# Kernel optimization log

Hardware: AMD Instinct MI355X
Metric: run time of the kernel (lower is better)

Reference implementation:

```python
import jax, jax.numpy as jnp
import numpy as np
import math
from jax import lax

_EPS = 1e-8


def _sinkhorn_uv(M, iters):
    # M: [BL, N, N] positive. Returns diagonal entries u, v of U, V such that
    # diag(u) @ M @ diag(v) is (approximately) doubly stochastic.
    u = jnp.ones(M.shape[:-1], M.dtype)  # [BL, N]
    v = jnp.ones(M.shape[:-1], M.dtype)  # [BL, N]
    def body(carry, _):
        u, v = carry
        u = 1.0 / (jnp.einsum('bij,bj->bi', M, v) + _EPS)
        v = 1.0 / (jnp.einsum('bij,bi->bj', M, u) + _EPS)
        return (u, v), None
    (u, v), _ = lax.scan(body, (u, v), None, length=iters)
    return u, v


def setup_inputs() -> dict:
    key = jax.random.key(0)
    k1, k2, k3, k4 = jax.random.split(key, 4)
    B, L, N, D = 2, 2048, 4, 2048
    nc = N * D
    nout = N * N + 2 * N
    h = jax.random.normal(k1, (B, L, N, D), dtype=jnp.float32)
    gamma = jnp.ones((nc,), dtype=jnp.float32)
    w = jax.random.normal(k2, (nc, nout), dtype=jnp.float32) * 0.02
    alpha = jnp.ones((3,), dtype=jnp.float32) * 0.01 + jax.random.uniform(k3, (3,)) * 0.01
    beta = jax.random.normal(k4, (nout,), dtype=jnp.float32) * 0.01
    return {"h": h, "gamma": gamma, "w": w, "alpha": alpha, "beta": beta, "max_sk_it": 10}


def reference(h, gamma, w, alpha, beta, max_sk_it):
    B, L, N, D = h.shape
    nc = N * D
    # --- mapping ---
    h_flat = h.reshape(B, L, nc)
    h_vec = gamma * h_flat                      # RMSNorm gamma scaling (module skips the division here)
    H = jnp.einsum('blc,co->blo', h_vec, w)     # [B, L, N^2 + 2N]
    r = jnp.linalg.norm(h_flat, axis=-1, keepdims=True) / math.sqrt(nc)
    r_ = 1.0 / r
    H_pre = jax.nn.sigmoid(r_ * H[..., :N] * alpha[0] + beta[:N])                 # [B,L,N]
    H_post = 2.0 * jax.nn.sigmoid(r_ * H[..., N:2 * N] * alpha[1] + beta[N:2 * N])  # [B,L,N]
    H_res_lin = r_ * H[..., 2 * N:] * alpha[2] + beta[2 * N:]                      # [B,L,N*N]
    M = jnp.exp(H_res_lin).reshape(B * L, N, N)
    u, v = _sinkhorn_uv(M, max_sk_it)
    u = lax.stop_gradient(u)
    v = lax.stop_gradient(v)
    P = u[:, :, None] * M * v[:, None, :]       # U @ M @ V with diagonal U, V
    H_res = P.reshape(B, L, N, N)
    # --- process ---
    h_pre = jnp.einsum('bln,blnd->bld', H_pre, h)        # [B,L,D]
    h_res = jnp.einsum('blmn,blnd->blmd', H_res, h)      # [B,L,N,D]
    # --- depth_connection (identity residual branch: h_out = h_pre) ---
    out = H_post[..., None] * h_pre[:, :, None, :] + h_res  # [B,L,N,D]
    return out
```

## Files before the change

kernel.cpp:

```cpp
#include <hip/hip_runtime.h>
#include <stdint.h>

#define NC       8192
#define D_       2048
#define NOUTS    24
#define WPAD     8224
#define NB       32
#define KW       512
#define LPAD     520

typedef __attribute__((ext_vector_type(8))) short short8;
typedef __attribute__((ext_vector_type(4))) float f32x4;

__device__ __forceinline__ uint16_t f32_to_bf16_bits(float f) {
    uint32_t u = __builtin_bit_cast(uint32_t, f);
    return (uint16_t)((u + 0x7FFFu + ((u >> 16) & 1u)) >> 16);
}


__global__ void prep_wb_kernel(const float* __restrict__ w,
                               const float* __restrict__ gamma,
                               uint16_t* __restrict__ wb) {
    int idx = blockIdx.x * blockDim.x + threadIdx.x;
    if (idx >= NB * NC) return;
    int o = idx / NC;
    int c = idx - o * NC;
    float v = (o < NOUTS) ? gamma[c] * w[c * NOUTS + o] : 0.0f;
    wb[o * NC + c] = f32_to_bf16_bits(v);
}

__global__ __launch_bounds__(256, 4) void gemv_mfma_lds_kernel(
    const float* __restrict__ h, const uint16_t* __restrict__ wb,
    float* __restrict__ part, int nrows)
{
    __shared__ __align__(16) uint16_t lwb[32][LPAD];

    const int tid  = threadIdx.x;
    const int lane = tid & 63;
    const int wid  = tid >> 6;
    const int nrg  = nrows >> 4;
    const int s    = (blockIdx.x * 4) / nrg;
    const int k0   = s * KW;

    {
        const int row = tid >> 3;
        const int col = (tid & 7) << 6;
        const uint16_t* src = wb + (size_t)row * NC + k0 + col;
        uint16_t* dst = &lwb[row][col];
#pragma unroll
        for (int i = 0; i < 8; ++i)
            *reinterpret_cast<uint4*>(dst + i * 8) =
                *reinterpret_cast<const uint4*>(src + i * 8);
    }
    __syncthreads();

    const int rg   = (blockIdx.x * 4 + wid) % nrg;
    const int r0   = rg * 16;
    const int arow = lane & 15;
    const int kgrp = (lane >> 4) << 3;
    const float*    hA  = h + (size_t)(r0 + arow) * NC + k0 + kgrp;
    const uint16_t* lB0 = &lwb[arow][kgrp];
    const uint16_t* lB1 = &lwb[arow + 16][kgrp];

    f32x4 acc0 = {0.f, 0.f, 0.f, 0.f};
    f32x4 acc1 = {0.f, 0.f, 0.f, 0.f};
    float ss = 0.0f;

#pragma unroll 8
    for (int k = 0; k < KW; k += 32) {
        const float4 a_lo = *reinterpret_cast<const float4*>(hA + k);
        const float4 a_hi = *reinterpret_cast<const float4*>(hA + k + 4);
        const short8 b0 = *reinterpret_cast<const short8*>(lB0 + k);
        const short8 b1 = *reinterpret_cast<const short8*>(lB1 + k);

        ss += a_lo.x*a_lo.x + a_lo.y*a_lo.y + a_lo.z*a_lo.z + a_lo.w*a_lo.w
            + a_hi.x*a_hi.x + a_hi.y*a_hi.y + a_hi.z*a_hi.z + a_hi.w*a_hi.w;

        short8 av;
        av[0] = (short)f32_to_bf16_bits(a_lo.x);
        av[1] = (short)f32_to_bf16_bits(a_lo.y);
        av[2] = (short)f32_to_bf16_bits(a_lo.z);
        av[3] = (short)f32_to_bf16_bits(a_lo.w);
        av[4] = (short)f32_to_bf16_bits(a_hi.x);
        av[5] = (short)f32_to_bf16_bits(a_hi.y);
        av[6] = (short)f32_to_bf16_bits(a_hi.z);
        av[7] = (short)f32_to_bf16_bits(a_hi.w);

        acc0 = __builtin_amdgcn_mfma_f32_16x16x32_bf16(av, b0, acc0, 0, 0, 0);
        acc1 = __builtin_amdgcn_mfma_f32_16x16x32_bf16(av, b1, acc1, 0, 0, 0);
    }

    ss += __shfl_xor(ss, 16, 64);
    ss += __shfl_xor(ss, 32, 64);

    const int o0   = lane & 15;
    const int crow = r0 + ((lane >> 4) << 2);
    float* pbase = part + (size_t)s * 25 * nrows;
#pragma unroll
    for (int i = 0; i < 4; ++i)
        pbase[(size_t)o0 * nrows + crow + i] = acc0[i];
    if (o0 < NOUTS - 16) {
#pragma unroll
        for (int i = 0; i < 4; ++i)
            pbase[(size_t)(o0 + 16) * nrows + crow + i] = acc1[i];
    }
    if (lane < 16)
        pbase[(size_t)24 * nrows + r0 + lane] = ss;
}

__global__ __launch_bounds__(256, 4) void gemv_mfma_kernel(
    const float* __restrict__ h, const uint16_t* __restrict__ wb,
    float* __restrict__ part, int nrows, int nslices)
{
    const int lane = threadIdx.x & 63;
    const int unit = blockIdx.x * 4 + (threadIdx.x >> 6);
    const int nrg  = nrows >> 4;
    const int rg   = unit % nrg;
    const int s    = unit / nrg;
    if (s >= nslices) return;
    const int r0 = rg * 16;
    const int kw = NC / nslices;
    const int k0 = s * kw;

    const int arow = lane & 15;
    const int kgrp = (lane >> 4) << 3;
    const float*    hA  = h  + (size_t)(r0 + arow) * NC + k0 + kgrp;
    const uint16_t* wB0 = wb + (size_t)arow        * NC + k0 + kgrp;
    const uint16_t* wB1 = wb + (size_t)(arow + 16) * NC + k0 + kgrp;

    f32x4 acc0 = {0.f, 0.f, 0.f, 0.f};
    f32x4 acc1 = {0.f, 0.f, 0.f, 0.f};
    float ss = 0.0f;

#pragma unroll 4
    for (int k = 0; k < kw; k += 32) {
        const float4 a_lo = *reinterpret_cast<const float4*>(hA + k);
        const float4 a_hi = *reinterpret_cast<const float4*>(hA + k + 4);
        const short8 b0 = *reinterpret_cast<const short8*>(wB0 + k);
        const short8 b1 = *reinterpret_cast<const short8*>(wB1 + k);

        ss += a_lo.x*a_lo.x + a_lo.y*a_lo.y + a_lo.z*a_lo.z + a_lo.w*a_lo.w
            + a_hi.x*a_hi.x + a_hi.y*a_hi.y + a_hi.z*a_hi.z + a_hi.w*a_hi.w;

        short8 av;
        av[0] = (short)f32_to_bf16_bits(a_lo.x);
        av[1] = (short)f32_to_bf16_bits(a_lo.y);
        av[2] = (short)f32_to_bf16_bits(a_lo.z);
        av[3] = (short)f32_to_bf16_bits(a_lo.w);
        av[4] = (short)f32_to_bf16_bits(a_hi.x);
        av[5] = (short)f32_to_bf16_bits(a_hi.y);
        av[6] = (short)f32_to_bf16_bits(a_hi.z);
        av[7] = (short)f32_to_bf16_bits(a_hi.w);

        acc0 = __builtin_amdgcn_mfma_f32_16x16x32_bf16(av, b0, acc0, 0, 0, 0);
        acc1 = __builtin_amdgcn_mfma_f32_16x16x32_bf16(av, b1, acc1, 0, 0, 0);
    }

    ss += __shfl_xor(ss, 16, 64);
    ss += __shfl_xor(ss, 32, 64);

    const int o0   = lane & 15;
    const int crow = r0 + ((lane >> 4) << 2);
    float* pbase = part + (size_t)s * 25 * nrows;
#pragma unroll
    for (int i = 0; i < 4; ++i)
        pbase[(size_t)o0 * nrows + crow + i] = acc0[i];
    if (o0 < NOUTS - 16) {
#pragma unroll
        for (int i = 0; i < 4; ++i)
            pbase[(size_t)(o0 + 16) * nrows + crow + i] = acc1[i];
    }
    if (lane < 16)
        pbase[(size_t)24 * nrows + r0 + lane] = ss;
}

__global__ void sinkhorn_wave_kernel(const float* __restrict__ part,
                                     const float* __restrict__ alpha,
                                     const float* __restrict__ beta,
                                     const int* __restrict__ it_ptr,
                                     float* __restrict__ Cbuf, int nrows, int nslices)
{
    const int lane = threadIdx.x & 63;
    const int row  = blockIdx.x * 4 + (threadIdx.x >> 6);
    if (row >= nrows) return;

    const int o = lane & 31;
    const int g = lane >> 5;
    float acc = 0.0f;
    if (o < 25) {
#pragma unroll 4
        for (int s = g; s < nslices; s += 2)
            acc += part[((size_t)s * 25 + o) * nrows + row];
    }
    acc += __shfl_xor(acc, 32, 64);

    float H[25];
#pragma unroll
    for (int i = 0; i < 25; ++i) H[i] = __shfl(acc, i, 64);

    const float r_ = sqrtf((float)NC / H[24]);
    const float a0 = alpha[0], a1 = alpha[1], a2 = alpha[2];

    float Hpre[4], Hpost[4], M[16];
#pragma unroll
    for (int n = 0; n < 4; ++n) {
        const float x = r_ * H[n] * a0 + beta[n];
        Hpre[n] = __builtin_amdgcn_rcpf(1.0f + __expf(-x));
        const float y = r_ * H[4 + n] * a1 + beta[4 + n];
        Hpost[n] = 2.0f * __builtin_amdgcn_rcpf(1.0f + __expf(-y));
    }
#pragma unroll
    for (int k = 0; k < 16; ++k)
        M[k] = __expf(r_ * H[8 + k] * a2 + beta[8 + k]);

    float u[4] = {1.f, 1.f, 1.f, 1.f}, vv[4] = {1.f, 1.f, 1.f, 1.f};
    int iters = *it_ptr;
    if (iters < 0 || iters > 10000) {
        const float f = __int_as_float(iters);
        iters = (f >= 0.0f && f < 10000.0f) ? (int)f : 10;
    }
    for (int it = 0; it < iters; ++it) {
#pragma unroll
        for (int i = 0; i < 4; ++i)
            u[i] = __builtin_amdgcn_rcpf(
                M[4*i+0]*vv[0] + M[4*i+1]*vv[1] + M[4*i+2]*vv[2] + M[4*i+3]*vv[3] + 1e-8f);
#pragma unroll
        for (int j2 = 0; j2 < 4; ++j2)
            vv[j2] = __builtin_amdgcn_rcpf(
                M[j2]*u[0] + M[4+j2]*u[1] + M[8+j2]*u[2] + M[12+j2]*u[3] + 1e-8f);
    }

    if (lane < 16) {
        const int m = lane >> 2, n = lane & 3;
        Cbuf[(size_t)row * 16 + lane] = Hpost[m] * Hpre[n] + u[m] * M[lane] * vv[n];
    }
}

__global__ __launch_bounds__(256, 8) void mix_kernel(
    const float* __restrict__ h, const float* __restrict__ Cbuf,
    float* __restrict__ out)
{
    const int row = blockIdx.x;
    const float* cr = Cbuf + (size_t)row * 16;
    float C[16];
#pragma unroll
    for (int k = 0; k < 16; ++k) C[k] = cr[k];

    const float* hr = h + (size_t)row * NC;
    float* orow = out + (size_t)row * NC;
#pragma unroll
    for (int t = 0; t < 2; ++t) {
        const int d0 = t * 1024 + (threadIdx.x << 2);
        float4 hn[4];
#pragma unroll
        for (int n = 0; n < 4; ++n)
            hn[n] = *reinterpret_cast<const float4*>(hr + n * D_ + d0);
#pragma unroll
        for (int m = 0; m < 4; ++m) {
            float4 o4;
            o4.x = C[4*m+0]*hn[0].x + C[4*m+1]*hn[1].x + C[4*m+2]*hn[2].x + C[4*m+3]*hn[3].x;
            o4.y = C[4*m+0]*hn[0].y + C[4*m+1]*hn[1].y + C[4*m+2]*hn[2].y + C[4*m+3]*hn[3].y;
            o4.z = C[4*m+0]*hn[0].z + C[4*m+1]*hn[1].z + C[4*m+2]*hn[2].z + C[4*m+3]*hn[3].z;
            o4.w = C[4*m+0]*hn[0].w + C[4*m+1]*hn[1].w + C[4*m+2]*hn[2].w + C[4*m+3]*hn[3].w;
            *reinterpret_cast<float4*>(orow + m * D_ + d0) = o4;
        }
    }
}


__global__ void prep_w_kernel(const float* __restrict__ w, float* __restrict__ wp) {
    int idx = blockIdx.x * blockDim.x + threadIdx.x;
    if (idx >= NOUTS * NC) return;
    int o = idx / NC;
    int c = idx - o * NC;
    wp[o * WPAD + c] = w[c * NOUTS + o];
}

__global__ __launch_bounds__(256, 4) void fused_kernel(
    const float* __restrict__ h, const float* __restrict__ gamma,
    const float* __restrict__ wp, const float* __restrict__ alpha,
    const float* __restrict__ beta, const int* __restrict__ it_ptr,
    float* __restrict__ out, int nrows)
{
    const int wave = threadIdx.x >> 6;
    const int lane = threadIdx.x & 63;
    const int row  = (blockIdx.x << 2) | wave;
    if (row >= nrows) return;
    const float* hrow = h + (size_t)row * NC;

    float acc[NOUTS];
#pragma unroll
    for (int o = 0; o < NOUTS; ++o) acc[o] = 0.0f;
    float sumsq = 0.0f;
    const int base = lane << 2;
#pragma unroll 2
    for (int j = 0; j < 32; ++j) {
        const int c0 = base + (j << 8);
        const float4 h4 = *reinterpret_cast<const float4*>(hrow + c0);
        const float4 g4 = *reinterpret_cast<const float4*>(gamma + c0);
        sumsq += h4.x*h4.x + h4.y*h4.y + h4.z*h4.z + h4.w*h4.w;
        const float v0 = h4.x*g4.x, v1 = h4.y*g4.y, v2 = h4.z*g4.z, v3 = h4.w*g4.w;
#pragma unroll
        for (int o = 0; o < NOUTS; ++o) {
            const float4 w4 = *reinterpret_cast<const float4*>(wp + o * WPAD + c0);
            acc[o] += v0*w4.x + v1*w4.y + v2*w4.z + v3*w4.w;
        }
    }
#pragma unroll
    for (int m = 1; m < 64; m <<= 1) {
        sumsq += __shfl_xor(sumsq, m, 64);
#pragma unroll
        for (int o = 0; o < NOUTS; ++o) acc[o] += __shfl_xor(acc[o], m, 64);
    }
    const float r_ = sqrtf((float)NC / sumsq);
    const float a0 = alpha[0], a1 = alpha[1], a2 = alpha[2];
    float Hpre[4], Hpost[4], M[16];
#pragma unroll
    for (int n = 0; n < 4; ++n) {
        const float x = r_ * acc[n] * a0 + beta[n];
        Hpre[n] = __builtin_amdgcn_rcpf(1.0f + __expf(-x));
        const float y = r_ * acc[4 + n] * a1 + beta[4 + n];
        Hpost[n] = 2.0f * __builtin_amdgcn_rcpf(1.0f + __expf(-y));
    }
#pragma unroll
    for (int k = 0; k < 16; ++k)
        M[k] = __expf(r_ * acc[8 + k] * a2 + beta[8 + k]);
    float u[4] = {1.f,1.f,1.f,1.f}, v[4] = {1.f,1.f,1.f,1.f};
    int iters = *it_ptr;
    if (iters < 0 || iters > 10000) {
        const float f = __int_as_float(iters);
        iters = (f >= 0.0f && f < 10000.0f) ? (int)f : 10;
    }
    for (int it = 0; it < iters; ++it) {
#pragma unroll
        for (int i = 0; i < 4; ++i)
            u[i] = __builtin_amdgcn_rcpf(M[4*i+0]*v[0] + M[4*i+1]*v[1] + M[4*i+2]*v[2] + M[4*i+3]*v[3] + 1e-8f);
#pragma unroll
        for (int j2 = 0; j2 < 4; ++j2)
            v[j2] = __builtin_amdgcn_rcpf(M[j2]*u[0] + M[4+j2]*u[1] + M[8+j2]*u[2] + M[12+j2]*u[3] + 1e-8f);
    }
    float P[16];
#pragma unroll
    for (int i = 0; i < 4; ++i)
#pragma unroll
        for (int j2 = 0; j2 < 4; ++j2)
            P[4*i + j2] = u[i] * M[4*i + j2] * v[j2];
    float* orow = out + (size_t)row * NC;
#pragma unroll 2
    for (int t = 0; t < 8; ++t) {
        const int d0 = base + (t << 8);
        float hn[4][4];
#pragma unroll
        for (int n = 0; n < 4; ++n) {
            const float4 x4 = *reinterpret_cast<const float4*>(hrow + n * D_ + d0);
            hn[n][0]=x4.x; hn[n][1]=x4.y; hn[n][2]=x4.z; hn[n][3]=x4.w;
        }
        float hp[4];
#pragma unroll
        for (int k = 0; k < 4; ++k)
            hp[k] = Hpre[0]*hn[0][k] + Hpre[1]*hn[1][k] + Hpre[2]*hn[2][k] + Hpre[3]*hn[3][k];
#pragma unroll
        for (int m = 0; m < 4; ++m) {
            float4 o4;
            o4.x = Hpost[m]*hp[0] + P[4*m+0]*hn[0][0] + P[4*m+1]*hn[1][0] + P[4*m+2]*hn[2][0] + P[4*m+3]*hn[3][0];
            o4.y = Hpost[m]*hp[1] + P[4*m+0]*hn[0][1] + P[4*m+1]*hn[1][1] + P[4*m+2]*hn[2][1] + P[4*m+3]*hn[3][1];
            o4.z = Hpost[m]*hp[2] + P[4*m+0]*hn[0][2] + P[4*m+1]*hn[1][2] + P[4*m+2]*hn[2][2] + P[4*m+3]*hn[3][2];
            o4.w = Hpost[m]*hp[3] + P[4*m+0]*hn[0][3] + P[4*m+1]*hn[1][3] + P[4*m+2]*hn[2][3] + P[4*m+3]*hn[3][3];
            *reinterpret_cast<float4*>(orow + m * D_ + d0) = o4;
        }
    }
}


extern "C" void kernel_launch(void* const* d_in, const int* in_sizes, int n_in,
                              void* d_out, int out_size, void* d_ws, size_t ws_size,
                              hipStream_t stream) {
    const float* h     = (const float*)d_in[0];
    const float* gamma = (const float*)d_in[1];
    const float* w     = (const float*)d_in[2];
    const float* alpha = (const float*)d_in[3];
    const float* beta  = (const float*)d_in[4];
    const int*   itp   = (const int*)d_in[5];
    float*       out   = (float*)d_out;

    const int nrows = in_sizes[0] / NC;

    const size_t wb_bytes = (size_t)NB * NC * 2;
    const size_t c_bytes  = (size_t)nrows * 16 * 4;

    int nslices = 0;
    if ((nrows % 16) == 0) {
        for (int cand = 16; cand >= 4; cand >>= 1) {
            const size_t pb = (size_t)cand * 25 * nrows * 4;
            if (ws_size >= wb_bytes + pb + c_bytes) { nslices = cand; break; }
        }
    }

    if (nslices) {
        uint16_t* wb   = (uint16_t*)d_ws;
        float*    part = (float*)((char*)d_ws + wb_bytes);
        float*    Cbuf = (float*)((char*)d_ws + wb_bytes + (size_t)nslices * 25 * nrows * 4);

        prep_wb_kernel<<<(NB * NC + 255) / 256, 256, 0, stream>>>(w, gamma, wb);
        if (nslices == 16 && (nrows % 64) == 0) {
            const int units = (nrows / 16) * 16;
            gemv_mfma_lds_kernel<<<units / 4, 256, 0, stream>>>(h, wb, part, nrows);
        } else {
            const int units = (nrows / 16) * nslices;
            gemv_mfma_kernel<<<(units + 3) / 4, 256, 0, stream>>>(h, wb, part, nrows, nslices);
        }
        sinkhorn_wave_kernel<<<(nrows + 3) / 4, 256, 0, stream>>>(part, alpha, beta, itp, Cbuf, nrows, nslices);
        mix_kernel<<<nrows, 256, 0, stream>>>(h, Cbuf, out);
    } else {
        float* wp = (float*)d_ws;
        prep_w_kernel<<<(NOUTS * NC + 255) / 256, 256, 0, stream>>>(w, wp);
        fused_kernel<<<(nrows + 3) / 4, 256, 0, stream>>>(h, gamma, wp, alpha, beta, itp, out, nrows);
    }
}
```

Measured before the change: 98.33 us.

## Fuse Sinkhorn coefficient computation into the mixing kernel per row

Merges the separate Sinkhorn kernel and the mix kernel into one kernel with one block per row. The first wave reduces the GEMV partials, runs Sinkhorn and writes the 16 mixing coefficients to shared memory. Meanwhile all threads have already issued their loads of h, which overlaps the h fetch with the Sinkhorn latency. This removes a kernel launch and the round trip of the coefficient buffer through global memory. In exchange, 63 of every 64 rows of Sinkhorn work sit behind a block-wide barrier, each block spends serial Sinkhorn time, and occupancy is reduced by register pressure.

```diff
diff --git a/kernel.cpp b/kernel.cpp
--- a/kernel.cpp
+++ b/kernel.cpp
@@ -174,96 +174,98 @@
         pbase[(size_t)24 * nrows + r0 + lane] = ss;
 }
 
-__global__ void sinkhorn_wave_kernel(const float* __restrict__ part,
-                                     const float* __restrict__ alpha,
-                                     const float* __restrict__ beta,
-                                     const int* __restrict__ it_ptr,
-                                     float* __restrict__ Cbuf, int nrows, int nslices)
+__global__ __launch_bounds__(256, 4) void sinkmix_kernel(
+    const float* __restrict__ h, const float* __restrict__ part,
+    const float* __restrict__ alpha, const float* __restrict__ beta,
+    const int* __restrict__ it_ptr, float* __restrict__ out,
+    int nrows, int nslices)
 {
-    const int lane = threadIdx.x & 63;
-    const int row  = blockIdx.x * 4 + (threadIdx.x >> 6);
-    if (row >= nrows) return;
-
-    const int o = lane & 31;
-    const int g = lane >> 5;
-    float acc = 0.0f;
-    if (o < 25) {
+    __shared__ float Cs[16];
+    const int row = blockIdx.x;
+    const int tid = threadIdx.x;
+    const float* hr = h + (size_t)row * NC;
+
+    const int d0 = tid << 2;
+    const int d1 = d0 + 1024;
+    float4 hA[4], hB[4];
+#pragma unroll
+    for (int n = 0; n < 4; ++n) {
+        hA[n] = *reinterpret_cast<const float4*>(hr + n * D_ + d0);
+        hB[n] = *reinterpret_cast<const float4*>(hr + n * D_ + d1);
+    }
+
+    if (tid < 64) {
+        const int o = tid & 31;
+        const int g = tid >> 5;
+        float acc = 0.0f;
+        if (o < 25) {
 #pragma unroll 4
-        for (int s = g; s < nslices; s += 2)
-            acc += part[((size_t)s * 25 + o) * nrows + row];
-    }
-    acc += __shfl_xor(acc, 32, 64);
-
-    float H[25];
-#pragma unroll
-    for (int i = 0; i < 25; ++i) H[i] = __shfl(acc, i, 64);
-
-    const float r_ = sqrtf((float)NC / H[24]);
-    const float a0 = alpha[0], a1 = alpha[1], a2 = alpha[2];
-
-    float Hpre[4], Hpost[4], M[16];
-#pragma unroll
-    for (int n = 0; n < 4; ++n) {
-        const float x = r_ * H[n] * a0 + beta[n];
-        Hpre[n] = __builtin_amdgcn_rcpf(1.0f + __expf(-x));
-        const float y = r_ * H[4 + n] * a1 + beta[4 + n];
-        Hpost[n] = 2.0f * __builtin_amdgcn_rcpf(1.0f + __expf(-y));
-    }
-#pragma unroll
-    for (int k = 0; k < 16; ++k)
-        M[k] = __expf(r_ * H[8 + k] * a2 + beta[8 + k]);
-
-    float u[4] = {1.f, 1.f, 1.f, 1.f}, vv[4] = {1.f, 1.f, 1.f, 1.f};
-    int iters = *it_ptr;
-    if (iters < 0 || iters > 10000) {
-        const float f = __int_as_float(iters);
-        iters = (f >= 0.0f && f < 10000.0f) ? (int)f : 10;
-    }
-    for (int it = 0; it < iters; ++it) {
-#pragma unroll
-        for (int i = 0; i < 4; ++i)
-            u[i] = __builtin_amdgcn_rcpf(
-                M[4*i+0]*vv[0] + M[4*i+1]*vv[1] + M[4*i+2]*vv[2] + M[4*i+3]*vv[3] + 1e-8f);
-#pragma unroll
-        for (int j2 = 0; j2 < 4; ++j2)
-            vv[j2] = __builtin_amdgcn_rcpf(
-                M[j2]*u[0] + M[4+j2]*u[1] + M[8+j2]*u[2] + M[12+j2]*u[3] + 1e-8f);
-    }
-
-    if (lane < 16) {
-        const int m = lane >> 2, n = lane & 3;
-        Cbuf[(size_t)row * 16 + lane] = Hpost[m] * Hpre[n] + u[m] * M[lane] * vv[n];
-    }
-}
-
-__global__ __launch_bounds__(256, 8) void mix_kernel(
-    const float* __restrict__ h, const float* __restrict__ Cbuf,
-    float* __restrict__ out)
-{
-    const int row = blockIdx.x;
-    const float* cr = Cbuf + (size_t)row * 16;
+            for (int s = g; s < nslices; s += 2)
+                acc += part[((size_t)s * 25 + o) * nrows + row];
+        }
+        acc += __shfl_xor(acc, 32, 64);
+
+        float H[25];
+#pragma unroll
+        for (int i = 0; i < 25; ++i) H[i] = __shfl(acc, i, 64);
+
+        const float r_ = sqrtf((float)NC / H[24]);
+        const float a0 = alpha[0], a1 = alpha[1], a2 = alpha[2];
+
+        float Hpre[4], Hpost[4], M[16];
+#pragma unroll
+        for (int n = 0; n < 4; ++n) {
+            const float x = r_ * H[n] * a0 + beta[n];
+            Hpre[n] = __builtin_amdgcn_rcpf(1.0f + __expf(-x));
+            const float y = r_ * H[4 + n] * a1 + beta[4 + n];
+            Hpost[n] = 2.0f * __builtin_amdgcn_rcpf(1.0f + __expf(-y));
+        }
+#pragma unroll
+        for (int k = 0; k < 16; ++k)
+            M[k] = __expf(r_ * H[8 + k] * a2 + beta[8 + k]);
+
+        float u[4] = {1.f, 1.f, 1.f, 1.f}, vv[4] = {1.f, 1.f, 1.f, 1.f};
+        int iters = *it_ptr;
+        if (iters < 0 || iters > 10000) {
+            const float f = __int_as_float(iters);
+            iters = (f >= 0.0f && f < 10000.0f) ? (int)f : 10;
+        }
+        for (int it = 0; it < iters; ++it) {
+#pragma unroll
+            for (int i = 0; i < 4; ++i)
+                u[i] = __builtin_amdgcn_rcpf(
+                    M[4*i+0]*vv[0] + M[4*i+1]*vv[1] + M[4*i+2]*vv[2] + M[4*i+3]*vv[3] + 1e-8f);
+#pragma unroll
+            for (int j2 = 0; j2 < 4; ++j2)
+                vv[j2] = __builtin_amdgcn_rcpf(
+                    M[j2]*u[0] + M[4+j2]*u[1] + M[8+j2]*u[2] + M[12+j2]*u[3] + 1e-8f);
+        }
+
+        if (tid < 16) {
+            const int m = tid >> 2, n = tid & 3;
+            Cs[tid] = Hpost[m] * Hpre[n] + u[m] * M[tid] * vv[n];
+        }
+    }
+    __syncthreads();
+
     float C[16];
 #pragma unroll
-    for (int k = 0; k < 16; ++k) C[k] = cr[k];
-
-    const float* hr = h + (size_t)row * NC;
+    for (int k = 0; k < 16; ++k) C[k] = Cs[k];
+
     float* orow = out + (size_t)row * NC;
 #pragma unroll
-    for (int t = 0; t < 2; ++t) {
-        const int d0 = t * 1024 + (threadIdx.x << 2);
-        float4 hn[4];
-#pragma unroll
-        for (int n = 0; n < 4; ++n)
-            hn[n] = *reinterpret_cast<const float4*>(hr + n * D_ + d0);
-#pragma unroll
-        for (int m = 0; m < 4; ++m) {
-            float4 o4;
-            o4.x = C[4*m+0]*hn[0].x + C[4*m+1]*hn[1].x + C[4*m+2]*hn[2].x + C[4*m+3]*hn[3].x;
-            o4.y = C[4*m+0]*hn[0].y + C[4*m+1]*hn[1].y + C[4*m+2]*hn[2].y + C[4*m+3]*hn[3].y;
-            o4.z = C[4*m+0]*hn[0].z + C[4*m+1]*hn[1].z + C[4*m+2]*hn[2].z + C[4*m+3]*hn[3].z;
-            o4.w = C[4*m+0]*hn[0].w + C[4*m+1]*hn[1].w + C[4*m+2]*hn[2].w + C[4*m+3]*hn[3].w;
-            *reinterpret_cast<float4*>(orow + m * D_ + d0) = o4;
-        }
+    for (int m = 0; m < 4; ++m) {
+        float4 oA, oB;
+        oA.x = C[4*m+0]*hA[0].x + C[4*m+1]*hA[1].x + C[4*m+2]*hA[2].x + C[4*m+3]*hA[3].x;
+        oA.y = C[4*m+0]*hA[0].y + C[4*m+1]*hA[1].y + C[4*m+2]*hA[2].y + C[4*m+3]*hA[3].y;
+        oA.z = C[4*m+0]*hA[0].z + C[4*m+1]*hA[1].z + C[4*m+2]*hA[2].z + C[4*m+3]*hA[3].z;
+        oA.w = C[4*m+0]*hA[0].w + C[4*m+1]*hA[1].w + C[4*m+2]*hA[2].w + C[4*m+3]*hA[3].w;
+        oB.x = C[4*m+0]*hB[0].x + C[4*m+1]*hB[1].x + C[4*m+2]*hB[2].x + C[4*m+3]*hB[3].x;
+        oB.y = C[4*m+0]*hB[0].y + C[4*m+1]*hB[1].y + C[4*m+2]*hB[2].y + C[4*m+3]*hB[3].y;
+        oB.z = C[4*m+0]*hB[0].z + C[4*m+1]*hB[1].z + C[4*m+2]*hB[2].z + C[4*m+3]*hB[3].z;
+        oB.w = C[4*m+0]*hB[0].w + C[4*m+1]*hB[1].w + C[4*m+2]*hB[2].w + C[4*m+3]*hB[3].w;
+        *reinterpret_cast<float4*>(orow + m * D_ + d0) = oA;
+        *reinterpret_cast<float4*>(orow + m * D_ + d1) = oB;
     }
 }
 
@@ -399,7 +401,6 @@
     if (nslices) {
         uint16_t* wb   = (uint16_t*)d_ws;
         float*    part = (float*)((char*)d_ws + wb_bytes);
-        float*    Cbuf = (float*)((char*)d_ws + wb_bytes + (size_t)nslices * 25 * nrows * 4);
 
         prep_wb_kernel<<<(NB * NC + 255) / 256, 256, 0, stream>>>(w, gamma, wb);
         if (nslices == 16 && (nrows % 64) == 0) {
@@ -409,8 +410,7 @@
             const int units = (nrows / 16) * nslices;
             gemv_mfma_kernel<<<(units + 3) / 4, 256, 0, stream>>>(h, wb, part, nrows, nslices);
         }
-        sinkhorn_wave_kernel<<<(nrows + 3) / 4, 256, 0, stream>>>(part, alpha, beta, itp, Cbuf, nrows, nslices);
-        mix_kernel<<<nrows, 256, 0, stream>>>(h, Cbuf, out);
+        sinkmix_kernel<<<nrows, 256, 0, stream>>>(h, part, alpha, beta, itp, out, nrows, nslices);
     } else {
         float* wp = (float*)d_ws;
         prep_w_kernel<<<(NOUTS * NC + 255) / 256, 256, 0, stream>>>(w, wp);
```

New measurement: 95.05 us. 1.03x faster.
